# Kernel optimization log

Hardware: AMD Instinct MI355X
Metric: run time of the kernel (lower is better)

Reference implementation:

```python
import jax, jax.numpy as jnp
import numpy as np

B, N, E2, D, H, L, DFC = 8, 1024, 128, 128, 4, 4, 128  # batch, nodes, 2*emb, hidden, heads, layers, fc dim


def setup_inputs() -> dict:
    key = jax.random.key(0)
    ks = jax.random.split(key, 12)
    def s(k, shape, fan):
        return jax.random.normal(k, shape, jnp.float32) / np.float32(np.sqrt(fan))
    x = jax.random.normal(ks[0], (B, N, E2), jnp.float32)
    u1 = jax.random.uniform(ks[1], (B, N, N), jnp.float32)
    u2 = jax.random.uniform(ks[2], (B, N, N), jnp.float32)
    adj1 = jnp.where(u1 > 0.95, u1, 0.0)  # weighted sparse adjacency
    adj2 = jnp.where(u2 > 0.95, u2, 0.0)
    valid = jnp.ones((B, N), jnp.float32)
    return {
        "x": x, "adj1": adj1, "adj2": adj2, "valid": valid,
        "W_embede": s(ks[3], (E2, D), E2),
        "Wh": s(ks[4], (L, D, D * H), D), "bh": jnp.zeros((L, D * H), jnp.float32),
        "We": s(ks[5], (L, D, D), D),
        "Wb": s(ks[6], (L, 2 * D, 1), 2 * D), "bb": jnp.zeros((L, 1), jnp.float32),
        "W_fc0": s(ks[7], (D, DFC), D), "b_fc0": jnp.zeros((DFC,), jnp.float32),
        "W_fcm": s(ks[8], (2, DFC, DFC), DFC), "b_fcm": jnp.zeros((2, DFC), jnp.float32),
        "W_fcl": s(ks[9], (DFC, 1), DFC), "b_fcl": jnp.zeros((1,), jnp.float32),
    }


def glema_layer(c, adj, Wh_k, bh_k, We_k, Wb_k, bb_k, nhop):
    # c: [B,N,D] -> h: [B,N,H,D]
    h = (c @ Wh_k + bh_k).reshape(B, N, H, D)
    e = jnp.einsum('bjil,bkil->bjik', h @ We_k, h)       # [B,N,H,N]
    e = e + jnp.transpose(e, (0, 3, 2, 1))               # undirected symmetrization
    mask = (adj > 0).astype(e.dtype)[:, :, None, :]
    att = jax.nn.softmax(e * mask, axis=1)               # softmax over source-node dim (as in torch)
    att = att * adj[:, :, None, :]
    z = h
    az = jax.nn.relu(jnp.einsum('biaj,bjak->biak', att, z))
    beta = jax.nn.sigmoid(jnp.concatenate([h, az], -1) @ Wb_k + bb_k)  # [B,N,H,1]
    for _ in range(nhop):
        az = jax.nn.relu(jnp.einsum('biaj,bjak->biak', att, z))
        z = beta * h + (1.0 - beta) * az
    return z.mean(-2)  # mean aggregation over heads -> [B,N,D]


def reference(x, adj1, adj2, valid, W_embede, Wh, bh, We, Wb, bb,
              W_fc0, b_fc0, W_fcm, b_fcm, W_fcl, b_fcl):
    c = x @ W_embede  # embede (no bias)
    for k in range(L):
        nhop = k + 1  # tactic == 'cont'
        c1 = glema_layer(c, adj1, Wh[k], bh[k], We[k], Wb[k], bb[k], nhop)
        c2 = glema_layer(c, adj2, Wh[k], bh[k], We[k], Wb[k], bb[k], nhop)
        c = c2 - c1  # branch == 'both'; dropout inactive (inference)
    c = c * valid[:, :, None]
    c = c.sum(1) / valid.sum(1, keepdims=True)  # [B,D]
    c = jax.nn.relu(c @ W_fc0 + b_fc0)
    for i in range(2):
        c = jax.nn.relu(c @ W_fcm[i] + b_fcm[i])
    c = jax.nn.sigmoid(c @ W_fcl + b_fcl)
    return c.reshape(-1)  # [B]
```

## Files before the change

### kernel.cpp

```cpp
#include <hip/hip_runtime.h>
#include <hip/hip_bf16.h>

#define BB 8
#define NN 1024
#define DD 128
#define HH 4
#define LL 4

typedef __attribute__((ext_vector_type(8))) short bf16x8;
typedef __attribute__((ext_vector_type(4))) float f32x4;
typedef __attribute__((ext_vector_type(8))) unsigned short u16x8;

__device__ __forceinline__ unsigned short f2bf(float f) {
  union { float f; unsigned int u; } v; v.f = f;
  unsigned int u = v.u;
  return (unsigned short)((u + 0x7FFFu + ((u >> 16) & 1u)) >> 16);
}
__device__ __forceinline__ float bf2f(unsigned short s) {
  union { unsigned int u; float f; } v; v.u = ((unsigned int)s) << 16;
  return v.f;
}
__device__ __forceinline__ float ubf_lo(unsigned int u) {
  union { unsigned int u; float f; } v; v.u = u << 16;
  return v.f;
}
__device__ __forceinline__ float ubf_hi(unsigned int u) {
  union { unsigned int u; float f; } v; v.u = u & 0xFFFF0000u;
  return v.f;
}
__device__ __forceinline__ unsigned short f2h(float f) {
  union { _Float16 h; unsigned short u; } v; v.h = (_Float16)f;
  return v.u;
}
__device__ __forceinline__ float h2f(unsigned short u) {
  union { unsigned short u; _Float16 h; } v; v.u = u;
  return (float)v.h;
}

__global__ __launch_bounds__(256) void k_maskT(const float* __restrict__ in,
                                               unsigned int* __restrict__ maskW) {
  __shared__ float t[32][33];
  int b = blockIdx.z;
  int x0 = blockIdx.x * 32, y0 = blockIdx.y * 32;
  int tx = threadIdx.x & 31, ty = threadIdx.x >> 5;
  const float* ib = in + (size_t)b * NN * NN;
#pragma unroll
  for (int j = 0; j < 32; j += 8)
    t[ty + j][tx] = ib[(size_t)(y0 + ty + j) * NN + x0 + tx];
  __syncthreads();
  const int half = (threadIdx.x >> 5) & 1;
#pragma unroll
  for (int j = 0; j < 32; j += 8) {
    bool nz = t[tx][ty + j] > 0.f;
    unsigned long long bl = __ballot(nz);
    unsigned int word = half ? (unsigned int)(bl >> 32) : (unsigned int)bl;
    if (tx == 0)
      maskW[((size_t)b * NN + x0 + ty + j) * 32 + (y0 >> 5)] = word;
  }
}

__global__ __launch_bounds__(256) void k_build(const float* __restrict__ adj,
                                               unsigned short* __restrict__ colidx,
                                               unsigned short* __restrict__ adjv,
                                               unsigned short* __restrict__ cnt) {
  const int b = blockIdx.y;
  const int wv = threadIdx.x >> 6, lane = threadIdx.x & 63;
  const int p = blockIdx.x * 4 + wv;
  const float* arow = adj + ((size_t)b * NN + p) * NN;
  const size_t base = ((size_t)b * NN + p) * 128;
  int run = 0;
  const unsigned long long lml = (lane == 63) ? 0x7FFFFFFFFFFFFFFFull
                                              : ((1ull << lane) - 1ull);
#pragma unroll
  for (int it = 0; it < 16; ++it) {
    float v = arow[it * 64 + lane];
    bool nz = v > 0.f;
    unsigned long long m = __ballot(nz);
    int pre = __popcll(m & lml);
    int slot = run + pre;
    if (nz && slot < 128) {
      colidx[base + slot] = (unsigned short)(it * 64 + lane);
      adjv[base + slot] = f2bf(v);
    }
    run += __popcll(m);
  }
  if (lane == 0) cnt[(size_t)b * NN + p] = (unsigned short)(run > 128 ? 128 : run);
}

__global__ __launch_bounds__(256) void k_wtrans(const float* __restrict__ in,
                                                unsigned short* __restrict__ out, int Nn) {
  __shared__ float t[32][33];
  int m = blockIdx.z;
  const float* ib = in + (size_t)m * 128 * Nn;
  unsigned short* ob = out + (size_t)m * Nn * 128;
  int k0 = blockIdx.x * 32, n0 = blockIdx.y * 32;
  int tx = threadIdx.x & 31, ty = threadIdx.x >> 5;
#pragma unroll
  for (int j = 0; j < 32; j += 8)
    t[ty + j][tx] = ib[(size_t)(k0 + ty + j) * Nn + n0 + tx];
  __syncthreads();
#pragma unroll
  for (int j = 0; j < 32; j += 8)
    ob[(size_t)(n0 + ty + j) * 128 + k0 + tx] = f2bf(t[tx][ty + j]);
}

__global__ __launch_bounds__(256) void k_gemm_k128(const float* __restrict__ A,
                                                   const float* __restrict__ Bw,
                                                   float* __restrict__ C,
                                                   unsigned short* __restrict__ Cbf,
                                                   int M, int Nn) {
  __shared__ __align__(16) float As[32][68];
  __shared__ __align__(16) float Bs[32][68];
  const int tm = blockIdx.x * 64, tn = blockIdx.y * 64;
  const int tid = threadIdx.x;
  const int ty = tid >> 4, tx = tid & 15;
  float acc[4][4] = {};
  for (int kc = 0; kc < 128; kc += 32) {
#pragma unroll
    for (int e = 0; e < 8; ++e) {
      int fl = tid + e * 256;
      int r = fl >> 5, k = fl & 31;
      As[k][r] = A[(size_t)(tm + r) * 128 + kc + k];
    }
#pragma unroll
    for (int e = 0; e < 8; ++e) {
      int fl = tid + e * 256;
      int k = fl >> 6, n = fl & 63;
      Bs[k][n] = Bw[(size_t)(kc + k) * Nn + tn + n];
    }
    __syncthreads();
#pragma unroll
    for (int kk = 0; kk < 32; ++kk) {
      float a4[4], b4[4];
      *(float4*)a4 = *(const float4*)&As[kk][ty * 4];
      *(float4*)b4 = *(const float4*)&Bs[kk][tx * 4];
#pragma unroll
      for (int i = 0; i < 4; ++i)
#pragma unroll
        for (int j = 0; j < 4; ++j) acc[i][j] += a4[i] * b4[j];
    }
    __syncthreads();
  }
#pragma unroll
  for (int i = 0; i < 4; ++i) {
    size_t base = (size_t)(tm + ty * 4 + i) * Nn + tn + tx * 4;
    *(float4*)&C[base] = *(float4*)acc[i];
    uint2 pv;
    pv.x = (unsigned int)f2bf(acc[i][0]) | ((unsigned int)f2bf(acc[i][1]) << 16);
    pv.y = (unsigned int)f2bf(acc[i][2]) | ((unsigned int)f2bf(acc[i][3]) << 16);
    *(uint2*)&Cbf[base] = pv;
  }
}

__global__ __launch_bounds__(256) void k_gemm_nt(const unsigned short* __restrict__ A,
                                                 const unsigned short* __restrict__ Bt,
                                                 const float* __restrict__ bias,
                                                 unsigned short* __restrict__ outp,
                                                 int Nn) {
  const int m0 = blockIdx.x * 64, n0 = blockIdx.y * 64;
  const int tid = threadIdx.x;
  const int wave = tid >> 6, lane = tid & 63;
  const int l15 = lane & 15, kq = lane >> 4;
  __shared__ __align__(16) unsigned short O[64][72];
  const unsigned short* aP = A + (size_t)(m0 + wave * 16 + l15) * 128;
  f32x4 acc[4] = {};
#pragma unroll
  for (int kk = 0; kk < 4; ++kk) {
    bf16x8 aF = *(const bf16x8*)(aP + (kk * 4 + kq) * 8);
#pragma unroll
    for (int cb = 0; cb < 4; ++cb) {
      bf16x8 bF = *(const bf16x8*)(Bt + (size_t)(n0 + cb * 16 + l15) * 128 + (kk * 4 + kq) * 8);
      acc[cb] = __builtin_amdgcn_mfma_f32_16x16x32_bf16(aF, bF, acc[cb], 0, 0, 0);
    }
  }
#pragma unroll
  for (int cb = 0; cb < 4; ++cb) {
    float bv = bias ? bias[n0 + cb * 16 + l15] : 0.f;
#pragma unroll
    for (int rg = 0; rg < 4; ++rg)
      O[wave * 16 + kq * 4 + rg][cb * 16 + l15] = f2bf(acc[cb][rg] + bv);
  }
  __syncthreads();
#pragma unroll
  for (int it = 0; it < 2; ++it) {
    int row = (tid >> 3) + it * 32, ch = tid & 7;
    *(uint4*)&outp[(size_t)(m0 + row) * Nn + n0 + ch * 8] = *(uint4*)&O[row][ch * 8];
  }
}

__global__ __launch_bounds__(256) void k_e_st(const unsigned short* __restrict__ g,
                                              const unsigned short* __restrict__ h,
                                              unsigned short* __restrict__ e, int b0) {
  const int t0 = blockIdx.x;
  int tr = (int)((sqrtf(8.f * t0 + 1.f) - 1.f) * 0.5f);
  while ((tr + 1) * (tr + 2) / 2 <= t0) ++tr;
  while (tr * (tr + 1) / 2 > t0) --tr;
  const int tp = t0 - tr * (tr + 1) / 2;
  const int gi = blockIdx.y;
  const int b = b0 + (gi >> 2), i = gi & 3;
  const int p0 = tp * 64, r0 = tr * 64;
  const bool diag = (tp == tr);
  __shared__ __align__(16) char lds[32768];
  const int tid = threadIdx.x;
  const unsigned short* gb = g + (size_t)b * NN * 512 + i * 128;
  const unsigned short* hb = h + (size_t)b * NN * 512 + i * 128;
#pragma unroll
  for (int e2 = 0; e2 < 8; ++e2) {
    int fl = tid + e2 * 256;
    int t = fl >> 10, rem = fl & 1023;
    int row = rem >> 4, ch = rem & 15;
    const unsigned short* src = t ? hb : gb;
    uint4 v = *(const uint4*)(src + (size_t)(r0 + row) * 512 + ch * 8);
    *(uint4*)(lds + t * 16384 + row * 256 + ((ch ^ (row & 7)) * 16)) = v;
  }
  __syncthreads();
  const int wave = tid >> 6, lane = tid & 63;
  const int l15 = lane & 15, kq = lane >> 4;
  const unsigned short* aG = gb + (size_t)(p0 + wave * 16 + l15) * 512;
  const unsigned short* aH = hb + (size_t)(p0 + wave * 16 + l15) * 512;
  f32x4 acc[4] = {};
#pragma unroll
  for (int kk = 0; kk < 4; ++kk) {
    bf16x8 gA = *(const bf16x8*)(aG + (kk * 4 + kq) * 8);
    bf16x8 hA = *(const bf16x8*)(aH + (kk * 4 + kq) * 8);
#pragma unroll
    for (int cb = 0; cb < 4; ++cb) {
      int row = cb * 16 + l15;
      int chs = ((kk * 4 + kq) ^ (row & 7)) * 16;
      bf16x8 gB = *(const bf16x8*)(lds + row * 256 + chs);
      bf16x8 hB = *(const bf16x8*)(lds + 16384 + row * 256 + chs);
      acc[cb] = __builtin_amdgcn_mfma_f32_16x16x32_bf16(gA, hB, acc[cb], 0, 0, 0);
      acc[cb] = __builtin_amdgcn_mfma_f32_16x16x32_bf16(hA, gB, acc[cb], 0, 0, 0);
    }
  }
  __syncthreads();
  unsigned short* eN = (unsigned short*)lds;
  unsigned short* eT = eN + 64 * 72;
#pragma unroll
  for (int cb = 0; cb < 4; ++cb)
#pragma unroll
    for (int rg = 0; rg < 4; ++rg) {
      const int pl = wave * 16 + kq * 4 + rg, rl = cb * 16 + l15;
      const unsigned short v = f2h(acc[cb][rg]);
      eN[pl * 72 + rl] = v;
      if (!diag) eT[rl * 72 + pl] = v;
    }
  __syncthreads();
  unsigned short* eb = e + (size_t)gi * NN * NN;
#pragma unroll
  for (int it = 0; it < 2; ++it) {
    const int row = (tid >> 3) + it * 32, ch = tid & 7;
    *(uint4*)&eb[(size_t)(p0 + row) * NN + r0 + ch * 8] = *(uint4*)&eN[row * 72 + ch * 8];
    if (!diag)
      *(uint4*)&eb[(size_t)(r0 + row) * NN + p0 + ch * 8] = *(uint4*)&eT[row * 72 + ch * 8];
  }
}

__global__ __launch_bounds__(128) void k_stats2(const unsigned short* __restrict__ e,
                                                const unsigned int* __restrict__ m1,
                                                const unsigned int* __restrict__ m2,
                                                float2* __restrict__ stats,
                                                size_t statsS, int b0) {
  const int col = blockIdx.x;
  const int r = col & (NN - 1);
  const int gi = col >> 10;
  const int b = b0 + (gi >> 2);
  const unsigned short* erow = e + (size_t)col * NN;
  const int tid = threadIdx.x;
  u16x8 ev = *(const u16x8*)(erow + tid * 8);
  float evf[8];
#pragma unroll
  for (int j = 0; j < 8; ++j) evf[j] = h2f((unsigned short)ev[j]);
  const size_t moff = ((size_t)b * NN + r) * 32 + (tid >> 2);
  const int sh = (tid & 3) * 8;
  unsigned int by1 = (m1[moff] >> sh) & 0xffu;
  unsigned int by2 = (m2[moff] >> sh) & 0xffu;
  float mx1 = 0.f, mx2 = 0.f;
#pragma unroll
  for (int j = 0; j < 8; ++j) {
    if ((by1 >> j) & 1u) mx1 = fmaxf(mx1, evf[j]);
    if ((by2 >> j) & 1u) mx2 = fmaxf(mx2, evf[j]);
  }
#pragma unroll
  for (int o = 32; o; o >>= 1) {
    mx1 = fmaxf(mx1, __shfl_xor(mx1, o));
    mx2 = fmaxf(mx2, __shfl_xor(mx2, o));
  }
  __shared__ float sm1[2], sm2[2], ss1[2], ss2[2];
  const int wv = tid >> 6, ln = tid & 63;
  if (ln == 0) { sm1[wv] = mx1; sm2[wv] = mx2; }
  __syncthreads();
  mx1 = fmaxf(sm1[0], sm1[1]);
  mx2 = fmaxf(sm2[0], sm2[1]);
  float ps1 = 0.f, ps2 = 0.f;
#pragma unroll
  for (int j = 0; j < 8; ++j) {
    float s1 = ((by1 >> j) & 1u) ? evf[j] : 0.f;
    float s2 = ((by2 >> j) & 1u) ? evf[j] : 0.f;
    ps1 += __expf(s1 - mx1);
    ps2 += __expf(s2 - mx2);
  }
#pragma unroll
  for (int o = 32; o; o >>= 1) {
    ps1 += __shfl_xor(ps1, o);
    ps2 += __shfl_xor(ps2, o);
  }
  if (ln == 0) { ss1[wv] = ps1; ss2[wv] = ps2; }
  __syncthreads();
  if (tid == 0) {
    const size_t gcol = (((size_t)gi + (size_t)b0 * HH) << 10) + r;
    stats[gcol] = make_float2(mx1, 1.f / (ss1[0] + ss1[1]));
    stats[statsS + gcol] = make_float2(mx2, 1.f / (ss2[0] + ss2[1]));
  }
}

__global__ __launch_bounds__(256) void k_attw2(const unsigned short* __restrict__ e,
                                               const unsigned short* __restrict__ cidxB,
                                               const unsigned short* __restrict__ adjvB,
                                               const unsigned short* __restrict__ cntB,
                                               size_t adjS, size_t cntS,
                                               const float2* __restrict__ stats,
                                               size_t statsS,
                                               unsigned int* __restrict__ att4,
                                               size_t attS, int b0) {
  const int br = blockIdx.z;
  const int gi = blockIdx.y;
  const int bl = gi >> 2, head = gi & 3;
  const int b = b0 + bl;
  const unsigned short* cidx = cidxB + (size_t)br * adjS;
  const unsigned short* adjv = adjvB + (size_t)br * adjS;
  const int wv = threadIdx.x >> 6, lane = threadIdx.x & 63;
  const int p = blockIdx.x * 4 + wv;
  const int n = cntB[(size_t)br * cntS + (size_t)b * NN + p];
  const int np4 = (n + 3) & ~3;
  const size_t cbase = ((size_t)b * NN + p) * 128;
  const unsigned short* erow = e + ((size_t)gi * NN + p) * NN;
  const float2* st = stats + (size_t)br * statsS + (((size_t)gi + (size_t)b0 * HH) << 10);
  unsigned int* ob = att4 + (size_t)br * attS + (((size_t)bl * NN + p) * 4 + head) * 128;
  for (int s = lane; s < np4; s += 64) {
    unsigned int o = 0;
    if (s < n) {
      int r = cidx[cbase + s];
      float2 mi = st[r];
      float val = __expf(h2f(erow[r]) - mi.x) * mi.y * bf2f(adjv[cbase + s]);
      o = ((unsigned int)r << 16) | (unsigned int)f2bf(val);
    }
    ob[s] = o;
  }
}

__global__ __launch_bounds__(256) void k_hwb(const unsigned short* __restrict__ h,
                                             const float* __restrict__ Wbk,
                                             float* __restrict__ hWb) {
  const int wid = threadIdx.x >> 6, lane = threadIdx.x & 63;
  const int idx = blockIdx.x * 4 + wid;
  const unsigned short* hp = h + (size_t)idx * 128;
  float s = 0.f;
#pragma unroll
  for (int e = 0; e < 2; ++e) {
    int d = lane + e * 64;
    s += bf2f(hp[d]) * Wbk[d];
  }
#pragma unroll
  for (int o = 32; o; o >>= 1) s += __shfl_xor(s, o);
  if (lane == 0) hWb[idx] = s;
}

template <int MODE>
__global__ __launch_bounds__(256) void k_az4(const unsigned int* __restrict__ att4,
                                             size_t attS,
                                             const unsigned short* __restrict__ cntB,
                                             size_t cntS,
                                             const unsigned short* __restrict__ zin,
                                             size_t zinS,
                                             const unsigned short* __restrict__ h,
                                             const float* __restrict__ hWb,
                                             const float* __restrict__ Wbk,
                                             const float* __restrict__ bbk,
                                             float* __restrict__ betaB, size_t betaS,
                                             unsigned short* __restrict__ outB,
                                             size_t outS, int b0) {
  const int br = blockIdx.z;
  const int bl = blockIdx.y;
  const int b = b0 + bl;
  const int wv = threadIdx.x >> 6, lane = threadIdx.x & 63;
  const int p = blockIdx.x * 4 + wv;
  const int head = lane >> 4;
  const int n = cntB[(size_t)br * cntS + (size_t)b * NN + p];
  const int np4 = (n + 3) & ~3;
  const unsigned int* ap =
      att4 + (size_t)br * attS + (((size_t)bl * NN + p) * 4 + head) * 128;
  const unsigned short* zbase = zin + (size_t)br * zinS + (size_t)b * NN * 512;
  const unsigned laneoff = (unsigned)lane * 8u;
  float a[8] = {};
  for (int s = 0; s < np4; s += 4) {
    uint4 aw = *(const uint4*)(ap + s);
    unsigned i0 = ((aw.x >> 7) & 0xFFFFFE00u) + laneoff;
    unsigned i1 = ((aw.y >> 7) & 0xFFFFFE00u) + laneoff;
    unsigned i2 = ((aw.z >> 7) & 0xFFFFFE00u) + laneoff;
    unsigned i3 = ((aw.w >> 7) & 0xFFFFFE00u) + laneoff;
    uint4 z0 = *(const uint4*)(zbase + i0);
    uint4 z1 = *(const uint4*)(zbase + i1);
    uint4 z2 = *(const uint4*)(zbase + i2);
    uint4 z3 = *(const uint4*)(zbase + i3);
    union { unsigned int u; float f; } c0, c1, c2, c3;
    c0.u = aw.x << 16; c1.u = aw.y << 16; c2.u = aw.z << 16; c3.u = aw.w << 16;
#define ACC8(zq, vv)                                            \
    a[0] += vv * ubf_lo(zq.x); a[1] += vv * ubf_hi(zq.x);       \
    a[2] += vv * ubf_lo(zq.y); a[3] += vv * ubf_hi(zq.y);       \
    a[4] += vv * ubf_lo(zq.z); a[5] += vv * ubf_hi(zq.z);       \
    a[6] += vv * ubf_lo(zq.w); a[7] += vv * ubf_hi(zq.w);
    ACC8(z0, c0.f) ACC8(z1, c1.f) ACC8(z2, c2.f) ACC8(z3, c3.f)
#undef ACC8
  }
#pragma unroll
  for (int j = 0; j < 8; ++j) a[j] = fmaxf(a[j], 0.f);
  const size_t gidx = ((size_t)b * NN + p) * HH + head;
  float bt;
  if (MODE == 0) {
    const float* wb2 = Wbk + 128 + (lane & 15) * 8;
    float part = 0.f;
#pragma unroll
    for (int j = 0; j < 8; ++j) part += a[j] * wb2[j];
    part += __shfl_xor(part, 1);
    part += __shfl_xor(part, 2);
    part += __shfl_xor(part, 4);
    part += __shfl_xor(part, 8);
    bt = 1.f / (1.f + __expf(-(hWb[gidx] + part + bbk[0])));
    if ((lane & 15) == 0) betaB[(size_t)br * betaS + gidx] = bt;
  } else {
    bt = betaB[(size_t)br * betaS + gidx];
  }
  const float om = 1.f - bt;
  const size_t obase = ((size_t)b * NN + p) * 512 + laneoff;
  uint4 hv = *(const uint4*)(h + obase);
  uint4 zo;
  zo.x = (unsigned int)f2bf(bt * ubf_lo(hv.x) + om * a[0]) |
         ((unsigned int)f2bf(bt * ubf_hi(hv.x) + om * a[1]) << 16);
  zo.y = (unsigned int)f2bf(bt * ubf_lo(hv.y) + om * a[2]) |
         ((unsigned int)f2bf(bt * ubf_hi(hv.y) + om * a[3]) << 16);
  zo.z = (unsigned int)f2bf(bt * ubf_lo(hv.z) + om * a[4]) |
         ((unsigned int)f2bf(bt * ubf_hi(hv.z) + om * a[5]) << 16);
  zo.w = (unsigned int)f2bf(bt * ubf_lo(hv.w) + om * a[6]) |
         ((unsigned int)f2bf(bt * ubf_hi(hv.w) + om * a[7]) << 16);
  *(uint4*)(outB + (size_t)br * outS + obase) = zo;
}

__global__ __launch_bounds__(256) void k_headmean2(const unsigned short* __restrict__ z1,
                                                   const unsigned short* __restrict__ z2,
                                                   float* __restrict__ outp,
                                                   unsigned short* __restrict__ outbf) {
  const int idx = blockIdx.x * 256 + threadIdx.x;
  const int d = idx & 127, bn = idx >> 7;
  const size_t base = (size_t)bn * 512 + d;
  float v1 = bf2f(z1[base]) + bf2f(z1[base + 128]) + bf2f(z1[base + 256]) + bf2f(z1[base + 384]);
  float v2 = bf2f(z2[base]) + bf2f(z2[base + 128]) + bf2f(z2[base + 256]) + bf2f(z2[base + 384]);
  float v = 0.25f * (v2 - v1);
  outp[idx] = v;
  outbf[idx] = f2bf(v);
}

__global__ __launch_bounds__(1024) void k_final2(const float* __restrict__ c,
                                                 const float* __restrict__ valid,
                                                 const float* __restrict__ Wfc0,
                                                 const float* __restrict__ bfc0,
                                                 const float* __restrict__ Wfcm,
                                                 const float* __restrict__ bfcm,
                                                 const float* __restrict__ Wfcl,
                                                 const float* __restrict__ bfcl,
                                                 float* __restrict__ out) {
  const int b = blockIdx.x, tid = threadIdx.x;
  const int ns = tid >> 7, d = tid & 127;
  __shared__ float red[8][128];
  __shared__ float vsh[8];
  __shared__ float bufA[128], bufB[128];
  float s = 0.f, vs = 0.f;
  const float* cb = c + ((size_t)b * NN + ns * 128) * 128 + d;
  const float* vb = valid + (size_t)b * NN + ns * 128;
  for (int n2 = 0; n2 < 128; ++n2) {
    float vv = vb[n2];
    s += cb[(size_t)n2 * 128] * vv;
    vs += vv;
  }
  red[ns][d] = s;
  if (d == 0) vsh[ns] = vs;
  __syncthreads();
  if (tid < 128) {
    float m = 0.f, vt = 0.f;
#pragma unroll
    for (int j = 0; j < 8; ++j) { m += red[j][tid]; vt += vsh[j]; }
    bufA[tid] = m / vt;
  }
  __syncthreads();
  if (tid < 128) {
    float t = bfc0[tid];
    for (int m = 0; m < 128; ++m) t += bufA[m] * Wfc0[m * 128 + tid];
    bufB[tid] = fmaxf(t, 0.f);
  }
  __syncthreads();
  if (tid < 128) {
    float t = bfcm[tid];
    for (int m = 0; m < 128; ++m) t += bufB[m] * Wfcm[m * 128 + tid];
    bufA[tid] = fmaxf(t, 0.f);
  }
  __syncthreads();
  if (tid < 128) {
    float t = bfcm[128 + tid];
    for (int m = 0; m < 128; ++m) t += bufA[m] * Wfcm[128 * 128 + m * 128 + tid];
    bufB[tid] = fmaxf(t, 0.f);
  }
  __syncthreads();
  if (tid < 128) red[0][tid] = bufB[tid] * Wfcl[tid];
  __syncthreads();
  if (tid < 64) red[0][tid] += red[0][tid + 64];
  __syncthreads();
  if (tid == 0) {
    float r = 0.f;
#pragma unroll
    for (int j = 0; j < 64; ++j) r += red[0][j];
    out[b] = 1.f / (1.f + __expf(-(r + bfcl[0])));
  }
}

extern "C" void kernel_launch(void* const* d_in, const int* in_sizes, int n_in,
                              void* d_out, int out_size, void* d_ws, size_t ws_size,
                              hipStream_t stream) {
  (void)in_sizes; (void)n_in; (void)out_size;
  const float* x     = (const float*)d_in[0];
  const float* adj1  = (const float*)d_in[1];
  const float* adj2  = (const float*)d_in[2];
  const float* valid = (const float*)d_in[3];
  const float* Wemb  = (const float*)d_in[4];
  const float* Wh    = (const float*)d_in[5];
  const float* bh    = (const float*)d_in[6];
  const float* We    = (const float*)d_in[7];
  const float* Wb    = (const float*)d_in[8];
  const float* bb    = (const float*)d_in[9];
  const float* Wfc0  = (const float*)d_in[10];
  const float* bfc0  = (const float*)d_in[11];
  const float* Wfcm  = (const float*)d_in[12];
  const float* bfcm  = (const float*)d_in[13];
  const float* Wfcl  = (const float*)d_in[14];
  const float* bfcl  = (const float*)d_in[15];
  float* out = (float*)d_out;

  const size_t adjS  = (size_t)BB * NN * 128;
  const size_t cntS  = (size_t)BB * NN;
  const size_t betaS = (size_t)BB * NN * HH;
  const size_t zS    = (size_t)BB * NN * HH * DD;
  const size_t statsS = (size_t)BB * HH * NN;

  float* w = (float*)d_ws;
  size_t off = 0;
  float* c    = w + off; off += (size_t)BB * NN * DD;
  float* beta = w + off; off += 2 * betaS;
  float2* stats = (float2*)(w + off); off += 2 * statsS * 2;
  float* hWb  = w + off; off += (size_t)BB * NN * HH;
  unsigned short* c_bf = (unsigned short*)(w + off); off += (size_t)BB * NN * DD / 2;
  unsigned short* h_bf = (unsigned short*)(w + off); off += (size_t)BB * NN * HH * DD / 2;
  unsigned short* g_bf = (unsigned short*)(w + off); off += (size_t)BB * NN * HH * DD / 2;
  unsigned short* zP0  = (unsigned short*)(w + off); off += 2 * zS / 2;
  unsigned short* zP1  = (unsigned short*)(w + off); off += 2 * zS / 2;
  unsigned short* WhT  = (unsigned short*)(w + off); off += (size_t)LL * 512 * 128 / 2;
  unsigned short* WeT  = (unsigned short*)(w + off); off += (size_t)LL * 128 * 128 / 2;
  unsigned int* maskT1 = (unsigned int*)(w + off); off += (size_t)BB * NN * 32;
  unsigned int* maskT2 = (unsigned int*)(w + off); off += (size_t)BB * NN * 32;
  unsigned short* cidxB = (unsigned short*)(w + off); off += 2 * adjS / 2;
  unsigned short* adjvB = (unsigned short*)(w + off); off += 2 * adjS / 2;
  unsigned short* cntB  = (unsigned short*)(w + off); off += (2 * cntS + 1) / 2;
  const size_t fixedF = off;
  const size_t eF = (size_t)HH * NN * NN / 2;
  const size_t aF = (size_t)HH * NN * 128;
  const size_t wsF = ws_size / sizeof(float);

  int G = 8;
  while (G > 1 && fixedF + (size_t)G * (eF + 2 * aF) > wsF) G >>= 1;

  unsigned short* e = (unsigned short*)(w + fixedF);
  unsigned int* att4 = (unsigned int*)(w + fixedF + (size_t)G * eF);
  const size_t attS = (size_t)G * NN * 512;

  k_maskT<<<dim3(32, 32, BB), 256, 0, stream>>>(adj1, maskT1);
  k_maskT<<<dim3(32, 32, BB), 256, 0, stream>>>(adj2, maskT2);
  k_build<<<dim3(256, BB), 256, 0, stream>>>(adj1, cidxB, adjvB, cntB);
  k_build<<<dim3(256, BB), 256, 0, stream>>>(adj2, cidxB + adjS, adjvB + adjS, cntB + cntS);
  k_wtrans<<<dim3(4, 16, LL), 256, 0, stream>>>(Wh, WhT, 512);
  k_wtrans<<<dim3(4, 4, LL), 256, 0, stream>>>(We, WeT, 128);
  k_gemm_k128<<<dim3(128, 2), 256, 0, stream>>>(x, Wemb, c, c_bf, BB * NN, DD);

  for (int k = 0; k < LL; ++k) {
    k_gemm_nt<<<dim3(128, 8), 256, 0, stream>>>(
        c_bf, WhT + (size_t)k * 512 * 128, bh + (size_t)k * 512, h_bf, 512);
    k_gemm_nt<<<dim3(512, 2), 256, 0, stream>>>(
        h_bf, WeT + (size_t)k * 128 * 128, nullptr, g_bf, 128);
    k_hwb<<<BB * NN * HH / 4, 256, 0, stream>>>(h_bf, Wb + (size_t)k * 2 * DD, hWb);
    for (int b0 = 0; b0 < BB; b0 += G) {
      k_e_st<<<dim3(136, G * HH), 256, 0, stream>>>(g_bf, h_bf, e, b0);
      k_stats2<<<G * HH * NN, 128, 0, stream>>>(e, maskT1, maskT2, stats, statsS, b0);
      k_attw2<<<dim3(256, G * HH, 2), 256, 0, stream>>>(
          e, cidxB, adjvB, cntB, adjS, cntS, stats, statsS, att4, attS, b0);
      k_az4<0><<<dim3(256, G, 2), 256, 0, stream>>>(
          att4, attS, cntB, cntS, h_bf, 0, h_bf, hWb,
          Wb + (size_t)k * 2 * DD, bb + k, beta, betaS, zP0, zS, b0);
      unsigned short *cur = zP0, *nxt = zP1;
      for (int t = 2; t <= k + 1; ++t) {
        k_az4<1><<<dim3(256, G, 2), 256, 0, stream>>>(
            att4, attS, cntB, cntS, cur, zS, h_bf, nullptr, nullptr, nullptr,
            beta, betaS, nxt, zS, b0);
        unsigned short* tm = cur; cur = nxt; nxt = tm;
      }
      const size_t oH = (size_t)b0 * NN * 512;
      const size_t oC = (size_t)b0 * NN * DD;
      k_headmean2<<<G * 512, 256, 0, stream>>>(
          cur + oH, cur + zS + oH, c + oC, c_bf + oC);
    }
  }
  k_final2<<<BB, 1024, 0, stream>>>(c, valid, Wfc0, bfc0, Wfcm, bfcm, Wfcl, bfcl, out);
}
```

Baseline: 1.033 ms.

## Pack four-head attention weights per edge and read column indices separately

```diff
diff --git a/kernel.cpp b/kernel.cpp
--- a/kernel.cpp
+++ b/kernel.cpp
@@ -84,7 +84,12 @@
     }
     run += __popcll(m);
   }
-  if (lane == 0) cnt[(size_t)b * NN + p] = (unsigned short)(run > 128 ? 128 : run);
+  const int nclamp = run > 128 ? 128 : run;
+  for (int s2 = nclamp + lane; s2 < 128; s2 += 64) {
+    colidx[base + s2] = 0;
+    adjv[base + s2] = 0;
+  }
+  if (lane == 0) cnt[(size_t)b * NN + p] = (unsigned short)nclamp;
 }
 
 __global__ __launch_bounds__(256) void k_wtrans(const float* __restrict__ in,
@@ -314,36 +319,42 @@
   }
 }
 
-__global__ __launch_bounds__(256) void k_attw2(const unsigned short* __restrict__ e,
+__global__ __launch_bounds__(256) void k_attw3(const unsigned short* __restrict__ e,
                                                const unsigned short* __restrict__ cidxB,
                                                const unsigned short* __restrict__ adjvB,
                                                const unsigned short* __restrict__ cntB,
                                                size_t adjS, size_t cntS,
                                                const float2* __restrict__ stats,
                                                size_t statsS,
-                                               unsigned int* __restrict__ att4,
-                                               size_t attS, int b0) {
+                                               uint2* __restrict__ attV,
+                                               size_t attVS, int b0) {
+  const int bl = blockIdx.x;
   const int br = blockIdx.z;
-  const int gi = blockIdx.y;
-  const int bl = gi >> 2, head = gi & 3;
   const int b = b0 + bl;
   const unsigned short* cidx = cidxB + (size_t)br * adjS;
   const unsigned short* adjv = adjvB + (size_t)br * adjS;
   const int wv = threadIdx.x >> 6, lane = threadIdx.x & 63;
-  const int p = blockIdx.x * 4 + wv;
+  const int p = blockIdx.y * 4 + wv;
   const int n = cntB[(size_t)br * cntS + (size_t)b * NN + p];
   const int np4 = (n + 3) & ~3;
   const size_t cbase = ((size_t)b * NN + p) * 128;
-  const unsigned short* erow = e + ((size_t)gi * NN + p) * NN;
-  const float2* st = stats + (size_t)br * statsS + (((size_t)gi + (size_t)b0 * HH) << 10);
-  unsigned int* ob = att4 + (size_t)br * attS + (((size_t)bl * NN + p) * 4 + head) * 128;
+  const unsigned short* ep = e + ((size_t)(bl * 4) * NN + p) * NN;
+  const float2* st = stats + (size_t)br * statsS + (((size_t)(bl * 4) + (size_t)b0 * HH) << 10);
+  uint2* ob = attV + (size_t)br * attVS + ((size_t)bl * NN + p) * 128;
   for (int s = lane; s < np4; s += 64) {
-    unsigned int o = 0;
+    uint2 o = make_uint2(0u, 0u);
     if (s < n) {
-      int r = cidx[cbase + s];
-      float2 mi = st[r];
-      float val = __expf(h2f(erow[r]) - mi.x) * mi.y * bf2f(adjv[cbase + s]);
-      o = ((unsigned int)r << 16) | (unsigned int)f2bf(val);
+      const int r = cidx[cbase + s];
+      const float av = bf2f(adjv[cbase + s]);
+      unsigned int v4[4];
+#pragma unroll
+      for (int hh = 0; hh < 4; ++hh) {
+        float2 mi = st[((size_t)hh << 10) + r];
+        float ev = h2f(ep[(size_t)hh * NN * NN + r]);
+        v4[hh] = (unsigned int)f2bf(__expf(ev - mi.x) * mi.y * av);
+      }
+      o.x = v4[0] | (v4[1] << 16);
+      o.y = v4[2] | (v4[3] << 16);
     }
     ob[s] = o;
   }
@@ -367,8 +378,10 @@
 }
 
 template <int MODE>
-__global__ __launch_bounds__(256) void k_az4(const unsigned int* __restrict__ att4,
-                                             size_t attS,
+__global__ __launch_bounds__(256) void k_az6(const uint2* __restrict__ attV,
+                                             size_t attVS,
+                                             const unsigned short* __restrict__ cidxB,
+                                             size_t adjS,
                                              const unsigned short* __restrict__ cntB,
                                              size_t cntS,
                                              const unsigned short* __restrict__ zin,
@@ -380,31 +393,37 @@
                                              float* __restrict__ betaB, size_t betaS,
                                              unsigned short* __restrict__ outB,
                                              size_t outS, int b0) {
+  const int bl = blockIdx.x;
   const int br = blockIdx.z;
-  const int bl = blockIdx.y;
   const int b = b0 + bl;
   const int wv = threadIdx.x >> 6, lane = threadIdx.x & 63;
-  const int p = blockIdx.x * 4 + wv;
+  const int p = blockIdx.y * 4 + wv;
   const int head = lane >> 4;
+  const int hshift = (head & 1) * 16;
   const int n = cntB[(size_t)br * cntS + (size_t)b * NN + p];
   const int np4 = (n + 3) & ~3;
-  const unsigned int* ap =
-      att4 + (size_t)br * attS + (((size_t)bl * NN + p) * 4 + head) * 128;
+  const unsigned short* cidx = cidxB + (size_t)br * adjS + ((size_t)b * NN + p) * 128;
+  const uint2* ap = attV + (size_t)br * attVS + ((size_t)bl * NN + p) * 128;
   const unsigned short* zbase = zin + (size_t)br * zinS + (size_t)b * NN * 512;
   const unsigned laneoff = (unsigned)lane * 8u;
   float a[8] = {};
   for (int s = 0; s < np4; s += 4) {
-    uint4 aw = *(const uint4*)(ap + s);
-    unsigned i0 = ((aw.x >> 7) & 0xFFFFFE00u) + laneoff;
-    unsigned i1 = ((aw.y >> 7) & 0xFFFFFE00u) + laneoff;
-    unsigned i2 = ((aw.z >> 7) & 0xFFFFFE00u) + laneoff;
-    unsigned i3 = ((aw.w >> 7) & 0xFFFFFE00u) + laneoff;
-    uint4 z0 = *(const uint4*)(zbase + i0);
-    uint4 z1 = *(const uint4*)(zbase + i1);
-    uint4 z2 = *(const uint4*)(zbase + i2);
-    uint4 z3 = *(const uint4*)(zbase + i3);
+    ushort4 rr = *(const ushort4*)(cidx + s);
+    uint4 v01 = *(const uint4*)(ap + s);
+    uint4 v23 = *(const uint4*)(ap + s + 2);
+    unsigned w0 = (head & 2) ? v01.y : v01.x;
+    unsigned w1 = (head & 2) ? v01.w : v01.z;
+    unsigned w2 = (head & 2) ? v23.y : v23.x;
+    unsigned w3 = (head & 2) ? v23.w : v23.z;
     union { unsigned int u; float f; } c0, c1, c2, c3;
-    c0.u = aw.x << 16; c1.u = aw.y << 16; c2.u = aw.z << 16; c3.u = aw.w << 16;
+    c0.u = (w0 >> hshift) << 16;
+    c1.u = (w1 >> hshift) << 16;
+    c2.u = (w2 >> hshift) << 16;
+    c3.u = (w3 >> hshift) << 16;
+    uint4 z0 = *(const uint4*)(zbase + (unsigned)rr.x * 512u + laneoff);
+    uint4 z1 = *(const uint4*)(zbase + (unsigned)rr.y * 512u + laneoff);
+    uint4 z2 = *(const uint4*)(zbase + (unsigned)rr.z * 512u + laneoff);
+    uint4 z3 = *(const uint4*)(zbase + (unsigned)rr.w * 512u + laneoff);
 #define ACC8(zq, vv)                                            \
     a[0] += vv * ubf_lo(zq.x); a[1] += vv * ubf_hi(zq.x);       \
     a[2] += vv * ubf_lo(zq.y); a[3] += vv * ubf_hi(zq.y);       \
@@ -570,15 +589,15 @@
   unsigned short* cntB  = (unsigned short*)(w + off); off += (2 * cntS + 1) / 2;
   const size_t fixedF = off;
   const size_t eF = (size_t)HH * NN * NN / 2;
-  const size_t aF = (size_t)HH * NN * 128;
+  const size_t aF = (size_t)NN * 128 * 2;
   const size_t wsF = ws_size / sizeof(float);
 
   int G = 8;
   while (G > 1 && fixedF + (size_t)G * (eF + 2 * aF) > wsF) G >>= 1;
 
   unsigned short* e = (unsigned short*)(w + fixedF);
-  unsigned int* att4 = (unsigned int*)(w + fixedF + (size_t)G * eF);
-  const size_t attS = (size_t)G * NN * 512;
+  uint2* attV = (uint2*)(w + fixedF + (size_t)G * eF);
+  const size_t attVS = (size_t)G * NN * 128;
 
   k_maskT<<<dim3(32, 32, BB), 256, 0, stream>>>(adj1, maskT1);
   k_maskT<<<dim3(32, 32, BB), 256, 0, stream>>>(adj2, maskT2);
@@ -597,16 +616,16 @@
     for (int b0 = 0; b0 < BB; b0 += G) {
       k_e_st<<<dim3(136, G * HH), 256, 0, stream>>>(g_bf, h_bf, e, b0);
       k_stats2<<<G * HH * NN, 128, 0, stream>>>(e, maskT1, maskT2, stats, statsS, b0);
-      k_attw2<<<dim3(256, G * HH, 2), 256, 0, stream>>>(
-          e, cidxB, adjvB, cntB, adjS, cntS, stats, statsS, att4, attS, b0);
-      k_az4<0><<<dim3(256, G, 2), 256, 0, stream>>>(
-          att4, attS, cntB, cntS, h_bf, 0, h_bf, hWb,
+      k_attw3<<<dim3(G, 256, 2), 256, 0, stream>>>(
+          e, cidxB, adjvB, cntB, adjS, cntS, stats, statsS, attV, attVS, b0);
+      k_az6<0><<<dim3(G, 256, 2), 256, 0, stream>>>(
+          attV, attVS, cidxB, adjS, cntB, cntS, h_bf, 0, h_bf, hWb,
           Wb + (size_t)k * 2 * DD, bb + k, beta, betaS, zP0, zS, b0);
       unsigned short *cur = zP0, *nxt = zP1;
       for (int t = 2; t <= k + 1; ++t) {
-        k_az4<1><<<dim3(256, G, 2), 256, 0, stream>>>(
-            att4, attS, cntB, cntS, cur, zS, h_bf, nullptr, nullptr, nullptr,
-            beta, betaS, nxt, zS, b0);
+        k_az6<1><<<dim3(G, 256, 2), 256, 0, stream>>>(
+            attV, attVS, cidxB, adjS, cntB, cntS, cur, zS, h_bf, nullptr, nullptr,
+            nullptr, beta, betaS, nxt, zS, b0);
         unsigned short* tm = cur; cur = nxt; nxt = tm;
       }
       const size_t oH = (size_t)b0 * NN * 512;
```

Measured after the change: 1.084 ms. +5.0%, slower.

## Switch intermediates from bf16 to fp16 and unroll sparse aggregation by eight

Applied to the files above, without the earlier changes.

```diff
diff --git a/kernel.cpp b/kernel.cpp
--- a/kernel.cpp
+++ b/kernel.cpp
@@ -7,7 +7,7 @@
 #define HH 4
 #define LL 4
 
-typedef __attribute__((ext_vector_type(8))) short bf16x8;
+typedef __attribute__((ext_vector_type(8))) _Float16 half8;
 typedef __attribute__((ext_vector_type(4))) float f32x4;
 typedef __attribute__((ext_vector_type(8))) unsigned short u16x8;
 
@@ -20,14 +20,6 @@
   union { unsigned int u; float f; } v; v.u = ((unsigned int)s) << 16;
   return v.f;
 }
-__device__ __forceinline__ float ubf_lo(unsigned int u) {
-  union { unsigned int u; float f; } v; v.u = u << 16;
-  return v.f;
-}
-__device__ __forceinline__ float ubf_hi(unsigned int u) {
-  union { unsigned int u; float f; } v; v.u = u & 0xFFFF0000u;
-  return v.f;
-}
 __device__ __forceinline__ unsigned short f2h(float f) {
   union { _Float16 h; unsigned short u; } v; v.h = (_Float16)f;
   return v.u;
@@ -35,6 +27,12 @@
 __device__ __forceinline__ float h2f(unsigned short u) {
   union { unsigned short u; _Float16 h; } v; v.u = u;
   return (float)v.h;
+}
+__device__ __forceinline__ half8 as_h8(uint4 u) {
+  union { uint4 u; half8 h; } v; v.u = u; return v.h;
+}
+__device__ __forceinline__ _Float16 lo16(unsigned int u) {
+  union { unsigned short s; _Float16 h; } v; v.s = (unsigned short)u; return v.h;
 }
 
 __global__ __launch_bounds__(256) void k_maskT(const float* __restrict__ in,
@@ -84,7 +82,12 @@
     }
     run += __popcll(m);
   }
-  if (lane == 0) cnt[(size_t)b * NN + p] = (unsigned short)(run > 128 ? 128 : run);
+  const int nclamp = run > 128 ? 128 : run;
+  for (int s2 = nclamp + lane; s2 < 128; s2 += 64) {
+    colidx[base + s2] = 0;
+    adjv[base + s2] = 0;
+  }
+  if (lane == 0) cnt[(size_t)b * NN + p] = (unsigned short)nclamp;
 }
 
 __global__ __launch_bounds__(256) void k_wtrans(const float* __restrict__ in,
@@ -101,7 +104,7 @@
   __syncthreads();
 #pragma unroll
   for (int j = 0; j < 32; j += 8)
-    ob[(size_t)(n0 + ty + j) * 128 + k0 + tx] = f2bf(t[tx][ty + j]);
+    ob[(size_t)(n0 + ty + j) * 128 + k0 + tx] = f2h(t[tx][ty + j]);
 }
 
 __global__ __launch_bounds__(256) void k_gemm_k128(const float* __restrict__ A,
@@ -146,8 +149,8 @@
     size_t base = (size_t)(tm + ty * 4 + i) * Nn + tn + tx * 4;
     *(float4*)&C[base] = *(float4*)acc[i];
     uint2 pv;
-    pv.x = (unsigned int)f2bf(acc[i][0]) | ((unsigned int)f2bf(acc[i][1]) << 16);
-    pv.y = (unsigned int)f2bf(acc[i][2]) | ((unsigned int)f2bf(acc[i][3]) << 16);
+    pv.x = (unsigned int)f2h(acc[i][0]) | ((unsigned int)f2h(acc[i][1]) << 16);
+    pv.y = (unsigned int)f2h(acc[i][2]) | ((unsigned int)f2h(acc[i][3]) << 16);
     *(uint2*)&Cbf[base] = pv;
   }
 }
@@ -166,11 +169,11 @@
   f32x4 acc[4] = {};
 #pragma unroll
   for (int kk = 0; kk < 4; ++kk) {
-    bf16x8 aF = *(const bf16x8*)(aP + (kk * 4 + kq) * 8);
+    half8 aF = *(const half8*)(aP + (kk * 4 + kq) * 8);
 #pragma unroll
     for (int cb = 0; cb < 4; ++cb) {
-      bf16x8 bF = *(const bf16x8*)(Bt + (size_t)(n0 + cb * 16 + l15) * 128 + (kk * 4 + kq) * 8);
-      acc[cb] = __builtin_amdgcn_mfma_f32_16x16x32_bf16(aF, bF, acc[cb], 0, 0, 0);
+      half8 bF = *(const half8*)(Bt + (size_t)(n0 + cb * 16 + l15) * 128 + (kk * 4 + kq) * 8);
+      acc[cb] = __builtin_amdgcn_mfma_f32_16x16x32_f16(aF, bF, acc[cb], 0, 0, 0);
     }
   }
 #pragma unroll
@@ -178,7 +181,7 @@
     float bv = bias ? bias[n0 + cb * 16 + l15] : 0.f;
 #pragma unroll
     for (int rg = 0; rg < 4; ++rg)
-      O[wave * 16 + kq * 4 + rg][cb * 16 + l15] = f2bf(acc[cb][rg] + bv);
+      O[wave * 16 + kq * 4 + rg][cb * 16 + l15] = f2h(acc[cb][rg] + bv);
   }
   __syncthreads();
 #pragma unroll
@@ -221,16 +224,16 @@
   f32x4 acc[4] = {};
 #pragma unroll
   for (int kk = 0; kk < 4; ++kk) {
-    bf16x8 gA = *(const bf16x8*)(aG + (kk * 4 + kq) * 8);
-    bf16x8 hA = *(const bf16x8*)(aH + (kk * 4 + kq) * 8);
+    half8 gA = *(const half8*)(aG + (kk * 4 + kq) * 8);
+    half8 hA = *(const half8*)(aH + (kk * 4 + kq) * 8);
 #pragma unroll
     for (int cb = 0; cb < 4; ++cb) {
       int row = cb * 16 + l15;
       int chs = ((kk * 4 + kq) ^ (row & 7)) * 16;
-      bf16x8 gB = *(const bf16x8*)(lds + row * 256 + chs);
-      bf16x8 hB = *(const bf16x8*)(lds + 16384 + row * 256 + chs);
-      acc[cb] = __builtin_amdgcn_mfma_f32_16x16x32_bf16(gA, hB, acc[cb], 0, 0, 0);
-      acc[cb] = __builtin_amdgcn_mfma_f32_16x16x32_bf16(hA, gB, acc[cb], 0, 0, 0);
+      half8 gB = *(const half8*)(lds + row * 256 + chs);
+      half8 hB = *(const half8*)(lds + 16384 + row * 256 + chs);
+      acc[cb] = __builtin_amdgcn_mfma_f32_16x16x32_f16(gA, hB, acc[cb], 0, 0, 0);
+      acc[cb] = __builtin_amdgcn_mfma_f32_16x16x32_f16(hA, gB, acc[cb], 0, 0, 0);
     }
   }
   __syncthreads();
@@ -314,7 +317,7 @@
   }
 }
 
-__global__ __launch_bounds__(256) void k_attw2(const unsigned short* __restrict__ e,
+__global__ __launch_bounds__(256) void k_attw4(const unsigned short* __restrict__ e,
                                                const unsigned short* __restrict__ cidxB,
                                                const unsigned short* __restrict__ adjvB,
                                                const unsigned short* __restrict__ cntB,
@@ -323,27 +326,28 @@
                                                size_t statsS,
                                                unsigned int* __restrict__ att4,
                                                size_t attS, int b0) {
+  const int bl = blockIdx.x;
   const int br = blockIdx.z;
-  const int gi = blockIdx.y;
-  const int bl = gi >> 2, head = gi & 3;
+  const int head = blockIdx.y >> 8, ptile = blockIdx.y & 255;
   const int b = b0 + bl;
+  const int gi = bl * HH + head;
   const unsigned short* cidx = cidxB + (size_t)br * adjS;
   const unsigned short* adjv = adjvB + (size_t)br * adjS;
   const int wv = threadIdx.x >> 6, lane = threadIdx.x & 63;
-  const int p = blockIdx.x * 4 + wv;
+  const int p = ptile * 4 + wv;
   const int n = cntB[(size_t)br * cntS + (size_t)b * NN + p];
-  const int np4 = (n + 3) & ~3;
+  const int np8 = (n + 7) & ~7;
   const size_t cbase = ((size_t)b * NN + p) * 128;
   const unsigned short* erow = e + ((size_t)gi * NN + p) * NN;
   const float2* st = stats + (size_t)br * statsS + (((size_t)gi + (size_t)b0 * HH) << 10);
   unsigned int* ob = att4 + (size_t)br * attS + (((size_t)bl * NN + p) * 4 + head) * 128;
-  for (int s = lane; s < np4; s += 64) {
+  for (int s = lane; s < np8; s += 64) {
     unsigned int o = 0;
     if (s < n) {
       int r = cidx[cbase + s];
       float2 mi = st[r];
       float val = __expf(h2f(erow[r]) - mi.x) * mi.y * bf2f(adjv[cbase + s]);
-      o = ((unsigned int)r << 16) | (unsigned int)f2bf(val);
+      o = ((unsigned int)r << 16) | (unsigned int)f2h(val);
     }
     ob[s] = o;
   }
@@ -359,7 +363,7 @@
 #pragma unroll
   for (int e = 0; e < 2; ++e) {
     int d = lane + e * 64;
-    s += bf2f(hp[d]) * Wbk[d];
+    s += h2f(hp[d]) * Wbk[d];
   }
 #pragma unroll
   for (int o = 32; o; o >>= 1) s += __shfl_xor(s, o);
@@ -367,7 +371,7 @@
 }
 
 template <int MODE>
-__global__ __launch_bounds__(256) void k_az4(const unsigned int* __restrict__ att4,
+__global__ __launch_bounds__(256) void k_az8(const unsigned int* __restrict__ att4,
                                              size_t attS,
                                              const unsigned short* __restrict__ cntB,
                                              size_t cntS,
@@ -380,37 +384,39 @@
                                              float* __restrict__ betaB, size_t betaS,
                                              unsigned short* __restrict__ outB,
                                              size_t outS, int b0) {
+  const int bl = blockIdx.x;
   const int br = blockIdx.z;
-  const int bl = blockIdx.y;
   const int b = b0 + bl;
   const int wv = threadIdx.x >> 6, lane = threadIdx.x & 63;
-  const int p = blockIdx.x * 4 + wv;
+  const int p = blockIdx.y * 4 + wv;
   const int head = lane >> 4;
   const int n = cntB[(size_t)br * cntS + (size_t)b * NN + p];
-  const int np4 = (n + 3) & ~3;
+  const int np8 = (n + 7) & ~7;
   const unsigned int* ap =
       att4 + (size_t)br * attS + (((size_t)bl * NN + p) * 4 + head) * 128;
   const unsigned short* zbase = zin + (size_t)br * zinS + (size_t)b * NN * 512;
   const unsigned laneoff = (unsigned)lane * 8u;
   float a[8] = {};
-  for (int s = 0; s < np4; s += 4) {
-    uint4 aw = *(const uint4*)(ap + s);
-    unsigned i0 = ((aw.x >> 7) & 0xFFFFFE00u) + laneoff;
-    unsigned i1 = ((aw.y >> 7) & 0xFFFFFE00u) + laneoff;
-    unsigned i2 = ((aw.z >> 7) & 0xFFFFFE00u) + laneoff;
-    unsigned i3 = ((aw.w >> 7) & 0xFFFFFE00u) + laneoff;
-    uint4 z0 = *(const uint4*)(zbase + i0);
-    uint4 z1 = *(const uint4*)(zbase + i1);
-    uint4 z2 = *(const uint4*)(zbase + i2);
-    uint4 z3 = *(const uint4*)(zbase + i3);
-    union { unsigned int u; float f; } c0, c1, c2, c3;
-    c0.u = aw.x << 16; c1.u = aw.y << 16; c2.u = aw.z << 16; c3.u = aw.w << 16;
-#define ACC8(zq, vv)                                            \
-    a[0] += vv * ubf_lo(zq.x); a[1] += vv * ubf_hi(zq.x);       \
-    a[2] += vv * ubf_lo(zq.y); a[3] += vv * ubf_hi(zq.y);       \
-    a[4] += vv * ubf_lo(zq.z); a[5] += vv * ubf_hi(zq.z);       \
-    a[6] += vv * ubf_lo(zq.w); a[7] += vv * ubf_hi(zq.w);
-    ACC8(z0, c0.f) ACC8(z1, c1.f) ACC8(z2, c2.f) ACC8(z3, c3.f)
+  for (int s = 0; s < np8; s += 8) {
+    uint4 awA = *(const uint4*)(ap + s);
+    uint4 awB = *(const uint4*)(ap + s + 4);
+    uint4 z0 = *(const uint4*)(zbase + (((awA.x >> 7) & 0xFFFFFE00u) + laneoff));
+    uint4 z1 = *(const uint4*)(zbase + (((awA.y >> 7) & 0xFFFFFE00u) + laneoff));
+    uint4 z2 = *(const uint4*)(zbase + (((awA.z >> 7) & 0xFFFFFE00u) + laneoff));
+    uint4 z3 = *(const uint4*)(zbase + (((awA.w >> 7) & 0xFFFFFE00u) + laneoff));
+    uint4 z4 = *(const uint4*)(zbase + (((awB.x >> 7) & 0xFFFFFE00u) + laneoff));
+    uint4 z5 = *(const uint4*)(zbase + (((awB.y >> 7) & 0xFFFFFE00u) + laneoff));
+    uint4 z6 = *(const uint4*)(zbase + (((awB.z >> 7) & 0xFFFFFE00u) + laneoff));
+    uint4 z7 = *(const uint4*)(zbase + (((awB.w >> 7) & 0xFFFFFE00u) + laneoff));
+#define ACC8(zq, aw)                                              \
+    {                                                             \
+      half8 zf = as_h8(zq);                                       \
+      float vf = (float)lo16(aw);                                 \
+      _Pragma("unroll")                                           \
+      for (int j = 0; j < 8; ++j) a[j] += vf * (float)zf[j];      \
+    }
+    ACC8(z0, awA.x) ACC8(z1, awA.y) ACC8(z2, awA.z) ACC8(z3, awA.w)
+    ACC8(z4, awB.x) ACC8(z5, awB.y) ACC8(z6, awB.z) ACC8(z7, awB.w)
 #undef ACC8
   }
 #pragma unroll
@@ -433,17 +439,16 @@
   }
   const float om = 1.f - bt;
   const size_t obase = ((size_t)b * NN + p) * 512 + laneoff;
-  uint4 hv = *(const uint4*)(h + obase);
-  uint4 zo;
-  zo.x = (unsigned int)f2bf(bt * ubf_lo(hv.x) + om * a[0]) |
-         ((unsigned int)f2bf(bt * ubf_hi(hv.x) + om * a[1]) << 16);
-  zo.y = (unsigned int)f2bf(bt * ubf_lo(hv.y) + om * a[2]) |
-         ((unsigned int)f2bf(bt * ubf_hi(hv.y) + om * a[3]) << 16);
-  zo.z = (unsigned int)f2bf(bt * ubf_lo(hv.z) + om * a[4]) |
-         ((unsigned int)f2bf(bt * ubf_hi(hv.z) + om * a[5]) << 16);
-  zo.w = (unsigned int)f2bf(bt * ubf_lo(hv.w) + om * a[6]) |
-         ((unsigned int)f2bf(bt * ubf_hi(hv.w) + om * a[7]) << 16);
-  *(uint4*)(outB + (size_t)br * outS + obase) = zo;
+  half8 hf = as_h8(*(const uint4*)(h + obase));
+  float zo[8];
+#pragma unroll
+  for (int j = 0; j < 8; ++j) zo[j] = bt * (float)hf[j] + om * a[j];
+  uint4 zv;
+  zv.x = (unsigned int)f2h(zo[0]) | ((unsigned int)f2h(zo[1]) << 16);
+  zv.y = (unsigned int)f2h(zo[2]) | ((unsigned int)f2h(zo[3]) << 16);
+  zv.z = (unsigned int)f2h(zo[4]) | ((unsigned int)f2h(zo[5]) << 16);
+  zv.w = (unsigned int)f2h(zo[6]) | ((unsigned int)f2h(zo[7]) << 16);
+  *(uint4*)(outB + (size_t)br * outS + obase) = zv;
 }
 
 __global__ __launch_bounds__(256) void k_headmean2(const unsigned short* __restrict__ z1,
@@ -453,11 +458,11 @@
   const int idx = blockIdx.x * 256 + threadIdx.x;
   const int d = idx & 127, bn = idx >> 7;
   const size_t base = (size_t)bn * 512 + d;
-  float v1 = bf2f(z1[base]) + bf2f(z1[base + 128]) + bf2f(z1[base + 256]) + bf2f(z1[base + 384]);
-  float v2 = bf2f(z2[base]) + bf2f(z2[base + 128]) + bf2f(z2[base + 256]) + bf2f(z2[base + 384]);
+  float v1 = h2f(z1[base]) + h2f(z1[base + 128]) + h2f(z1[base + 256]) + h2f(z1[base + 384]);
+  float v2 = h2f(z2[base]) + h2f(z2[base + 128]) + h2f(z2[base + 256]) + h2f(z2[base + 384]);
   float v = 0.25f * (v2 - v1);
   outp[idx] = v;
-  outbf[idx] = f2bf(v);
+  outbf[idx] = f2h(v);
 }
 
 __global__ __launch_bounds__(1024) void k_final2(const float* __restrict__ c,
@@ -570,7 +575,7 @@
   unsigned short* cntB  = (unsigned short*)(w + off); off += (2 * cntS + 1) / 2;
   const size_t fixedF = off;
   const size_t eF = (size_t)HH * NN * NN / 2;
-  const size_t aF = (size_t)HH * NN * 128;
+  const size_t aF = (size_t)NN * 512;
   const size_t wsF = ws_size / sizeof(float);
 
   int G = 8;
@@ -597,14 +602,14 @@
     for (int b0 = 0; b0 < BB; b0 += G) {
       k_e_st<<<dim3(136, G * HH), 256, 0, stream>>>(g_bf, h_bf, e, b0);
       k_stats2<<<G * HH * NN, 128, 0, stream>>>(e, maskT1, maskT2, stats, statsS, b0);
-      k_attw2<<<dim3(256, G * HH, 2), 256, 0, stream>>>(
+      k_attw4<<<dim3(G, 1024, 2), 256, 0, stream>>>(
           e, cidxB, adjvB, cntB, adjS, cntS, stats, statsS, att4, attS, b0);
-      k_az4<0><<<dim3(256, G, 2), 256, 0, stream>>>(
+      k_az8<0><<<dim3(G, 256, 2), 256, 0, stream>>>(
           att4, attS, cntB, cntS, h_bf, 0, h_bf, hWb,
           Wb + (size_t)k * 2 * DD, bb + k, beta, betaS, zP0, zS, b0);
       unsigned short *cur = zP0, *nxt = zP1;
       for (int t = 2; t <= k + 1; ++t) {
-        k_az4<1><<<dim3(256, G, 2), 256, 0, stream>>>(
+        k_az8<1><<<dim3(G, 256, 2), 256, 0, stream>>>(
             att4, attS, cntB, cntS, cur, zS, h_bf, nullptr, nullptr, nullptr,
             beta, betaS, nxt, zS, b0);
         unsigned short* tm = cur; cur = nxt; nxt = tm;
```

Result: faster. 1.004 ms (-2.8%).
